# Optimization experiments

Measured on AMD Instinct MI355X. Metric: run time of the kernel, lower is better.

The kernel has to match this reference:

```python
import jax, jax.numpy as jnp
import numpy as np

NUM_HEADS = 12


def setup_inputs() -> dict:
    key = jax.random.key(0)
    ks = jax.random.split(key, 7)
    B, H, W, C = 1, 64, 64, 768
    hd = C // NUM_HEADS
    return {
        "x": jax.random.normal(ks[0], (B, H, W, C), dtype=jnp.float32),
        "qkv_w": jax.random.normal(ks[1], (C, 3 * C), dtype=jnp.float32) * 0.02,
        "qkv_b": jax.random.normal(ks[2], (3 * C,), dtype=jnp.float32) * 0.02,
        "proj_w": jax.random.normal(ks[3], (C, C), dtype=jnp.float32) * 0.02,
        "proj_b": jax.random.normal(ks[4], (C,), dtype=jnp.float32) * 0.02,
        "rel_pos_h": jax.random.normal(ks[5], (2 * H - 1, hd), dtype=jnp.float32) * 0.02,
        "rel_pos_w": jax.random.normal(ks[6], (2 * W - 1, hd), dtype=jnp.float32) * 0.02,
    }


def _rel_table(size, rel_pos):
    # q_size == k_size so relative_coords = i - j + (size - 1)
    coords = jnp.arange(size)[:, None] - jnp.arange(size)[None, :] + (size - 1)
    return rel_pos[coords]  # [size, size, head_dim]


def reference(x, qkv_w, qkv_b, proj_w, proj_b, rel_pos_h, rel_pos_w):
    B, H, W, C = x.shape
    nh = NUM_HEADS
    hd = C // nh
    scale = hd ** -0.5
    N = H * W

    qkv = x.reshape(B, N, C) @ qkv_w + qkv_b  # [B, N, 3C]
    qkv = qkv.reshape(B, N, 3, nh, hd).transpose(2, 0, 3, 1, 4).reshape(3, B * nh, N, hd)
    q, k, v = qkv[0], qkv[1], qkv[2]

    attn = jnp.einsum("bqd,bkd->bqk", q * scale, k)  # [B*nh, N, N]

    # decomposed relative position bias
    Rh = _rel_table(H, rel_pos_h)  # [H, H, hd]
    Rw = _rel_table(W, rel_pos_w)  # [W, W, hd]
    qr = q.reshape(B * nh, H, W, hd)
    rel_h = jnp.einsum("bhwc,hkc->bhwk", qr, Rh)  # [B*nh, H, W, H]
    rel_w = jnp.einsum("bhwc,wkc->bhwk", qr, Rw)  # [B*nh, H, W, W]
    bias = rel_h[..., :, None] + rel_w[..., None, :]  # [B*nh, H, W, H, W]
    attn = attn + bias.reshape(B * nh, N, N)

    attn = jax.nn.softmax(attn, axis=-1)
    out = jnp.einsum("bqk,bkd->bqd", attn, v)  # [B*nh, N, hd]
    out = out.reshape(B, nh, H, W, hd).transpose(0, 2, 3, 1, 4).reshape(B, H, W, C)
    return out @ proj_w + proj_b
```

## Files before the change

kernel.cpp:

```cpp
#include <hip/hip_runtime.h>
#include <math.h>

#define NHEADS 12
#define NTOK 4096
#define LOG2E 1.44269504f

typedef __attribute__((ext_vector_type(8))) short bf8v;
typedef __attribute__((ext_vector_type(4))) float f4v;
typedef __attribute__((ext_vector_type(16))) float f16v;

__device__ __forceinline__ unsigned short f2bf(float f) {
  unsigned int u = __float_as_uint(f);
  u += 0x7fffu + ((u >> 16) & 1u);
  return (unsigned short)(u >> 16);
}
__device__ __forceinline__ bf8v pack8(float4 a, float4 b) {
  bf8v v;
  v[0] = (short)f2bf(a.x); v[1] = (short)f2bf(a.y);
  v[2] = (short)f2bf(a.z); v[3] = (short)f2bf(a.w);
  v[4] = (short)f2bf(b.x); v[5] = (short)f2bf(b.y);
  v[6] = (short)f2bf(b.z); v[7] = (short)f2bf(b.w);
  return v;
}
__device__ __forceinline__ unsigned cvtpk(float lo, float hi) {
  unsigned r;
  asm("v_cvt_pk_bf16_f32 %0, %1, %2" : "=v"(r) : "v"(lo), "v"(hi));
  return r;
}
__device__ __forceinline__ void gload_lds16(const void* g, void* l) {
  __builtin_amdgcn_global_load_lds(
      (const __attribute__((address_space(1))) void*)g,
      (__attribute__((address_space(3))) void*)l, 16, 0, 0);
}

__device__ __forceinline__ void tcvt_body(
    const float* __restrict__ in, short* __restrict__ out, int R, int C,
    int bx, int by, int t, float (*Ts)[65])
{
    const int bc = bx * 64, br = by * 64;
    {
        const int r = t >> 2, c0 = (t & 3) * 16;
        const float* src = in + (size_t)(br + r) * C + bc + c0;
#pragma unroll
        for (int i = 0; i < 4; ++i) {
            float4 a = *(const float4*)(src + 4 * i);
            Ts[r][c0 + 4 * i + 0] = a.x;
            Ts[r][c0 + 4 * i + 1] = a.y;
            Ts[r][c0 + 4 * i + 2] = a.z;
            Ts[r][c0 + 4 * i + 3] = a.w;
        }
    }
    __syncthreads();
    const int c = t >> 2, r0 = (t & 3) * 16;
    short* dst = out + (size_t)(bc + c) * R + br + r0;
#pragma unroll
    for (int p = 0; p < 2; ++p) {
        bf8v v;
#pragma unroll
        for (int i = 0; i < 8; ++i) v[i] = (short)f2bf(Ts[r0 + p * 8 + i][c]);
        *(bf8v*)(dst + p * 8) = v;
    }
}

__global__ __launch_bounds__(256) void prep_kernel(
    const float* __restrict__ x, const float* __restrict__ qkvw,
    const float* __restrict__ pw, short* __restrict__ xh,
    short* __restrict__ wqkvT, short* __restrict__ pwT)
{
    __shared__ float Ts[64][65];
    const int bid = blockIdx.x, t = threadIdx.x;
    if (bid < 1536) {
        const size_t i = ((size_t)bid * 256 + t) * 8;
        float4 a = *(const float4*)(x + i);
        float4 b = *(const float4*)(x + i + 4);
        *(bf8v*)(xh + i) = pack8(a, b);
    } else if (bid < 1968) {
        const int idx = bid - 1536;
        tcvt_body(qkvw, wqkvT, 768, 2304, idx % 36, idx / 36, t, Ts);
    } else {
        const int idx = bid - 1968;
        tcvt_body(pw, pwT, 768, 768, idx % 12, idx / 12, t, Ts);
    }
}

__global__ __launch_bounds__(256) void qkv_mfma_kernel(
    const short* __restrict__ xh, const short* __restrict__ wT,
    const float* __restrict__ bias, short* __restrict__ qbh,
    short* __restrict__ kblk, short* __restrict__ vblk)
{
    __shared__ __align__(16) short As[128 * 32];
    __shared__ __align__(16) short Bs[96 * 32];
    const int t = threadIdx.x;
    const int w = t >> 6, lane = t & 63;
    const int l15 = lane & 15, l4 = lane >> 4;
    const int wr = w >> 1, wc = w & 1;
    const int row0 = blockIdx.y * 128, col0 = blockIdx.x * 96;
    const int ldr = lane >> 2;
    const int ldk = (lane & 3) * 8;

    f4v acc[4][3] = {};
    const short* aBase = xh + (size_t)(row0 + w * 32 + ldr) * 768 + ldk;
    const short* bBase0 = wT + (size_t)(col0 + w * 16 + ldr) * 768 + ldk;
    const short* bBase1 = wT + (size_t)(col0 + 64 + w * 16 + ldr) * 768 + ldk;

    for (int kk = 0; kk < 768; kk += 32) {
        __syncthreads();
#pragma unroll
        for (int c = 0; c < 2; ++c)
            gload_lds16(aBase + (size_t)c * 16 * 768 + kk,
                        &As[(w * 32 + c * 16) * 32]);
        gload_lds16(bBase0 + kk, &Bs[(w * 16) * 32]);
        if (w < 2)
            gload_lds16(bBase1 + kk, &Bs[(64 + w * 16) * 32]);
        __syncthreads();
        bf8v af[4], bg[3];
#pragma unroll
        for (int i = 0; i < 4; ++i)
            af[i] = *(const bf8v*)&As[(wr * 64 + 16 * i + l15) * 32 + l4 * 8];
#pragma unroll
        for (int j = 0; j < 3; ++j)
            bg[j] = *(const bf8v*)&Bs[(wc * 48 + 16 * j + l15) * 32 + l4 * 8];
#pragma unroll
        for (int i = 0; i < 4; ++i)
#pragma unroll
            for (int j = 0; j < 3; ++j)
                acc[i][j] = __builtin_amdgcn_mfma_f32_16x16x32_bf16(
                    af[i], bg[j], acc[i][j], 0, 0, 0);
    }

#pragma unroll
    for (int j = 0; j < 3; ++j) {
        const int n = col0 + wc * 48 + 16 * j + l15;
        const int s = n / 768;
        const int rm = n - s * 768;
        const int h = rm >> 6, d = rm & 63;
        const float bv = bias[n];
        if (s == 2) {
#pragma unroll
            for (int i = 0; i < 4; ++i) {
                const int m = row0 + wr * 64 + 16 * i + l4 * 4;
                short4 pv;
                pv.x = (short)f2bf(acc[i][j][0] + bv);
                pv.y = (short)f2bf(acc[i][j][1] + bv);
                pv.z = (short)f2bf(acc[i][j][2] + bv);
                pv.w = (short)f2bf(acc[i][j][3] + bv);
                *(short4*)(vblk +
                           ((size_t)(h * 256 + (m >> 4)) * 64 + d) * 16 +
                           (m & 15)) = pv;
            }
        } else if (s == 0) {
#pragma unroll
            for (int i = 0; i < 4; ++i) {
                const int m = row0 + wr * 64 + 16 * i + l4 * 4;
#pragma unroll
                for (int r = 0; r < 4; ++r)
                    qbh[((size_t)h * NTOK + m + r) * 64 + d] =
                        (short)f2bf(acc[i][j][r] + bv);
            }
        } else {
#pragma unroll
            for (int i = 0; i < 4; ++i) {
                const int m = row0 + wr * 64 + 16 * i + l4 * 4;
                short* dst = kblk +
                    ((((size_t)(h * 128 + (m >> 5)) * 8 + (d >> 3)) * 32 +
                      (m & 31)) * 8 + (d & 7));
#pragma unroll
                for (int r = 0; r < 4; ++r)
                    dst[r * 8] = (short)f2bf(acc[i][j][r] + bv);
            }
        }
    }
}

union FlashSMem {
    float relHs[64][65];
    float U[128 * 65];
    struct {
        float OEp[64][64];
        float lEp[64];
    };
};

__global__ __launch_bounds__(256, 3) void flash_mfma_kernel(
    const short* __restrict__ qbh, const short* __restrict__ kblk,
    const short* __restrict__ vblk, const float* __restrict__ rpw,
    const float* __restrict__ rph, short* __restrict__ aob)
{
    __shared__ __align__(16) FlashSMem sm;

    const int t = threadIdx.x;
    const int qt = blockIdx.x, head = blockIdx.y;
    const int row0 = qt * 64;
    const int lane = t & 63, w = t >> 6;
    const int qh2 = w & 1, th = w >> 1;
    const int l31 = lane & 31, hf = lane >> 5;
    const size_t hB = (size_t)head * NTOK * 64;
    const float SC = 0.125f * LOG2E;

    const int q = row0 + qh2 * 32 + l31;
    bf8v bQ[4];
    {
        const short* qsrc = qbh + hB + (size_t)q * 64;
#pragma unroll
        for (int ks = 0; ks < 4; ++ks)
            bQ[ks] = *(const bf8v*)(qsrc + ks * 16 + hf * 8);
    }

    const short* kb = kblk + (size_t)head * 262144 + th * 4096 + hf * 256 +
                      (size_t)l31 * 8;
    bf8v kf[2][4];
#pragma unroll
    for (int t32 = 0; t32 < 2; ++t32)
#pragma unroll
        for (int ks = 0; ks < 4; ++ks)
            kf[t32][ks] = *(const bf8v*)(kb + t32 * 2048 + ks * 512);

    const short* vb2 = vblk + ((size_t)head * 256 * 64 + l31) * 16 + hf * 8;

#pragma unroll
    for (int jt2 = 0; jt2 < 2; ++jt2) {
        const int jt = 2 * th + jt2;
        int j = jt * 32 + l31;
        if (j > 126) j = 0;
        const float* asrc = rpw + (size_t)j * 64;
        f16v c = {};
#pragma unroll
        for (int ks = 0; ks < 4; ++ks) {
            float4 u0 = *(const float4*)(asrc + ks * 16 + hf * 8);
            float4 u1 = *(const float4*)(asrc + ks * 16 + hf * 8 + 4);
            c = __builtin_amdgcn_mfma_f32_32x32x16_bf16(
                pack8(u0, u1), bQ[ks], c, 0, 0, 0);
        }
#pragma unroll
        for (int reg = 0; reg < 16; ++reg)
            sm.U[(jt * 32 + (reg & 3) + 8 * (reg >> 2) + 4 * hf) * 65 +
                 qh2 * 32 + l31] = c[reg];
    }
    __syncthreads();
    const int qw = qh2 * 32 + l31;
    float rwf[2][4][4];
#pragma unroll
    for (int t32 = 0; t32 < 2; ++t32)
#pragma unroll
        for (int g = 0; g < 4; ++g) {
            const int kw = t32 * 32 + 8 * g + 4 * hf;
#pragma unroll
            for (int e = 0; e < 4; ++e)
                rwf[t32][g][e] =
                    sm.U[(qw + 63 - kw - e) * 65 + qw] * LOG2E;
        }
    __syncthreads();

    {
        const int kh = th * 32 + l31;
        const float* asrc = rph + (size_t)(qt + 63 - kh) * 64;
        f16v c = {};
#pragma unroll
        for (int ks = 0; ks < 4; ++ks) {
            float4 u0 = *(const float4*)(asrc + ks * 16 + hf * 8);
            float4 u1 = *(const float4*)(asrc + ks * 16 + hf * 8 + 4);
            u0.x *= LOG2E; u0.y *= LOG2E; u0.z *= LOG2E; u0.w *= LOG2E;
            u1.x *= LOG2E; u1.y *= LOG2E; u1.z *= LOG2E; u1.w *= LOG2E;
            c = __builtin_amdgcn_mfma_f32_32x32x16_bf16(
                pack8(u0, u1), bQ[ks], c, 0, 0, 0);
        }
#pragma unroll
        for (int reg = 0; reg < 16; ++reg)
            sm.relHs[th * 32 + (reg & 3) + 8 * (reg >> 2) + 4 * hf]
                    [qh2 * 32 + l31] = c[reg];
    }
    __syncthreads();

    f16v O[2] = {{}, {}};
    float lsum = 0.f;

    for (int it = 0; it < 32; ++it) {
        f16v acc[2] = {{}, {}};
#pragma unroll
        for (int ks = 0; ks < 4; ++ks)
#pragma unroll
            for (int t32 = 0; t32 < 2; ++t32)
                acc[t32] = __builtin_amdgcn_mfma_f32_32x32x16_bf16(
                    kf[t32][ks], bQ[ks], acc[t32], 0, 0, 0);

        {
            const int itn = (it < 31) ? it + 1 : 31;
            const short* kp = kb + (size_t)itn * 8192;
#pragma unroll
            for (int t32 = 0; t32 < 2; ++t32)
#pragma unroll
                for (int ks = 0; ks < 4; ++ks)
                    kf[t32][ks] =
                        *(const bf8v*)(kp + t32 * 2048 + ks * 512);
        }

        bf8v vB[2][2][2];
        {
            const short* vit = vb2 + (size_t)(it * 8 + th * 4) * 64 * 16;
#pragma unroll
            for (int t32 = 0; t32 < 2; ++t32)
#pragma unroll
                for (int ks2 = 0; ks2 < 2; ++ks2)
#pragma unroll
                    for (int nt = 0; nt < 2; ++nt)
                        vB[t32][ks2][nt] = *(const bf8v*)(
                            vit + ((size_t)(t32 * 2 + ks2) * 64 + nt * 32) *
                                      16);
        }

        const float rh = sm.relHs[2 * it + th][qw];

        unsigned xg[2][4], yg[2][4];
#pragma unroll
        for (int t32 = 0; t32 < 2; ++t32) {
            float sub = 0.f;
#pragma unroll
            for (int g = 0; g < 4; ++g) {
                const float e0 = __builtin_amdgcn_exp2f(
                    fmaf(acc[t32][4 * g + 0], SC, rwf[t32][g][0] + rh));
                const float e1 = __builtin_amdgcn_exp2f(
                    fmaf(acc[t32][4 * g + 1], SC, rwf[t32][g][1] + rh));
                const float e2 = __builtin_amdgcn_exp2f(
                    fmaf(acc[t32][4 * g + 2], SC, rwf[t32][g][2] + rh));
                const float e3 = __builtin_amdgcn_exp2f(
                    fmaf(acc[t32][4 * g + 3], SC, rwf[t32][g][3] + rh));
                sub += (e0 + e1) + (e2 + e3);
                xg[t32][g] = cvtpk(e0, e1);
                yg[t32][g] = cvtpk(e2, e3);
            }
            lsum += sub;
        }

#pragma unroll
        for (int t32 = 0; t32 < 2; ++t32)
#pragma unroll
            for (int ks2 = 0; ks2 < 2; ++ks2) {
                auto px = __builtin_amdgcn_permlane32_swap(
                    xg[t32][2 * ks2], xg[t32][2 * ks2 + 1], false, false);
                auto py = __builtin_amdgcn_permlane32_swap(
                    yg[t32][2 * ks2], yg[t32][2 * ks2 + 1], false, false);
                int4 av;
                av.x = (int)px[0];
                av.y = (int)py[0];
                av.z = (int)px[1];
                av.w = (int)py[1];
                union { int4 i; bf8v v; } u; u.i = av;
#pragma unroll
                for (int nt = 0; nt < 2; ++nt)
                    O[nt] = __builtin_amdgcn_mfma_f32_32x32x16_bf16(
                        u.v, vB[t32][ks2][nt], O[nt], 0, 0, 0);
            }
    }

    lsum += __shfl_xor(lsum, 32);
    __syncthreads();
    if (th == 1) {
#pragma unroll
        for (int nt = 0; nt < 2; ++nt)
#pragma unroll
            for (int reg = 0; reg < 16; ++reg) {
                const int qr = (reg & 3) + 8 * (reg >> 2) + 4 * hf;
                sm.OEp[qh2 * 32 + qr][nt * 32 + l31] = O[nt][reg];
            }
        if (lane < 32) sm.lEp[qh2 * 32 + l31] = lsum;
    }
    __syncthreads();
    if (th == 0) {
        lsum += sm.lEp[qh2 * 32 + l31];
        const float linv = 1.0f / lsum;
#pragma unroll
        for (int nt = 0; nt < 2; ++nt)
#pragma unroll
            for (int reg = 0; reg < 16; ++reg) {
                const int qr = (reg & 3) + 8 * (reg >> 2) + 4 * hf;
                const float li = __shfl(linv, qr);
                const float o =
                    O[nt][reg] + sm.OEp[qh2 * 32 + qr][nt * 32 + l31];
                aob[(size_t)(row0 + qh2 * 32 + qr) * 768 + head * 64 +
                    nt * 32 + l31] = (short)f2bf(o * li);
            }
    }
}

__global__ __launch_bounds__(256) void proj_mfma_kernel(
    const short* __restrict__ aoh, const short* __restrict__ pwT,
    const float* __restrict__ bias, float* __restrict__ out)
{
    __shared__ __align__(16) short As[64 * 32];
    __shared__ __align__(16) short Bs[128 * 32];
    const int t = threadIdx.x;
    const int w = t >> 6, lane = t & 63;
    const int l15 = lane & 15, l4 = lane >> 4;
    const int wr = w >> 1, wc = w & 1;
    const int row0 = blockIdx.y * 64, col0 = blockIdx.x * 128;
    const int ldr = lane >> 2;
    const int ldk = (lane & 3) * 8;

    f4v acc[2][4] = {};
    const short* aBase = aoh + (size_t)(row0 + w * 16 + ldr) * 768 + ldk;
    const short* bBase = pwT + (size_t)(col0 + w * 32 + ldr) * 768 + ldk;

    for (int kk = 0; kk < 768; kk += 32) {
        __syncthreads();
        gload_lds16(aBase + kk, &As[(w * 16) * 32]);
#pragma unroll
        for (int c = 0; c < 2; ++c)
            gload_lds16(bBase + (size_t)c * 16 * 768 + kk,
                        &Bs[(w * 32 + c * 16) * 32]);
        __syncthreads();
        bf8v af[2], bg[4];
#pragma unroll
        for (int i = 0; i < 2; ++i)
            af[i] = *(const bf8v*)&As[(wr * 32 + 16 * i + l15) * 32 + l4 * 8];
#pragma unroll
        for (int j = 0; j < 4; ++j)
            bg[j] = *(const bf8v*)&Bs[(wc * 64 + 16 * j + l15) * 32 + l4 * 8];
#pragma unroll
        for (int i = 0; i < 2; ++i)
#pragma unroll
            for (int j = 0; j < 4; ++j)
                acc[i][j] = __builtin_amdgcn_mfma_f32_16x16x32_bf16(
                    af[i], bg[j], acc[i][j], 0, 0, 0);
    }

#pragma unroll
    for (int j = 0; j < 4; ++j) {
        const int n = col0 + wc * 64 + 16 * j + l15;
        const float bv = bias[n];
#pragma unroll
        for (int i = 0; i < 2; ++i) {
            const int m = row0 + wr * 32 + 16 * i + l4 * 4;
#pragma unroll
            for (int r = 0; r < 4; ++r)
                out[(size_t)(m + r) * 768 + n] = acc[i][j][r] + bv;
        }
    }
}

extern "C" void kernel_launch(void* const* d_in, const int* in_sizes, int n_in,
                              void* d_out, int out_size, void* d_ws,
                              size_t ws_size, hipStream_t stream)
{
    (void)in_sizes; (void)n_in; (void)out_size; (void)ws_size;
    const float* x    = (const float*)d_in[0];
    const float* qkvw = (const float*)d_in[1];
    const float* qkvb = (const float*)d_in[2];
    const float* pw   = (const float*)d_in[3];
    const float* pb   = (const float*)d_in[4];
    const float* rph  = (const float*)d_in[5];
    const float* rpw  = (const float*)d_in[6];
    float* out = (float*)d_out;

    const size_t S = (size_t)NHEADS * NTOK * 64;
    short* qbh  = (short*)d_ws;
    short* kblk = qbh + S;
    short* vblk = kblk + S;
    short* xh   = vblk + S;
    short* aob  = xh;
    short* wqkvT = xh + S;
    short* pwT  = wqkvT + (size_t)2304 * 768;

    prep_kernel<<<dim3(2112), 256, 0, stream>>>(x, qkvw, pw, xh, wqkvT, pwT);
    qkv_mfma_kernel<<<dim3(24, 32), 256, 0, stream>>>(xh, wqkvT, qkvb,
                                                      qbh, kblk, vblk);
    flash_mfma_kernel<<<dim3(64, NHEADS), 256, 0, stream>>>(qbh, kblk, vblk,
                                                            rpw, rph, aob);
    proj_mfma_kernel<<<dim3(6, 64), 256, 0, stream>>>(aob, pwT, pb, out);
}
```

Measured before the change: 217.9 us.

## Pack rel-pos-w bias to bf16 pairs, reorder K prefetch, halve proj tile width

The per-lane relative-position-W bias registers in the flash kernel are now stored as packed bf16 pairs, which halves their register footprint, and are unpacked with shifts and masks in the inner loop. The next-iteration K fragment prefetch moves after the V loads. The projection GEMM tile shrinks from 64x128 to 64x64, doubling the grid to fill more CUs. The bias packing lowers the precision of the rel-w bias and adds ALU work per score.

After: 212.1 us. 1.03x faster.

```diff
diff --git a/kernel.cpp b/kernel.cpp
--- a/kernel.cpp
+++ b/kernel.cpp
@@ -21,6 +21,10 @@
   v[4] = (short)f2bf(b.x); v[5] = (short)f2bf(b.y);
   v[6] = (short)f2bf(b.z); v[7] = (short)f2bf(b.w);
   return v;
+}
+__device__ __forceinline__ unsigned pkbf(float hi, float lo) {
+  return __builtin_amdgcn_perm(__float_as_uint(hi) + 0x8000u,
+                               __float_as_uint(lo) + 0x8000u, 0x07060302u);
 }
 __device__ __forceinline__ unsigned cvtpk(float lo, float hi) {
   unsigned r;
@@ -238,16 +242,18 @@
     }
     __syncthreads();
     const int qw = qh2 * 32 + l31;
-    float rwf[2][4][4];
+    uint2 rwp[2][4];
 #pragma unroll
     for (int t32 = 0; t32 < 2; ++t32)
 #pragma unroll
         for (int g = 0; g < 4; ++g) {
             const int kw = t32 * 32 + 8 * g + 4 * hf;
-#pragma unroll
-            for (int e = 0; e < 4; ++e)
-                rwf[t32][g][e] =
-                    sm.U[(qw + 63 - kw - e) * 65 + qw] * LOG2E;
+            const float v0 = sm.U[(qw + 63 - kw) * 65 + qw] * LOG2E;
+            const float v1 = sm.U[(qw + 62 - kw) * 65 + qw] * LOG2E;
+            const float v2 = sm.U[(qw + 61 - kw) * 65 + qw] * LOG2E;
+            const float v3 = sm.U[(qw + 60 - kw) * 65 + qw] * LOG2E;
+            rwp[t32][g].x = pkbf(v1, v0);
+            rwp[t32][g].y = pkbf(v3, v2);
         }
     __syncthreads();
 
@@ -283,17 +289,6 @@
                 acc[t32] = __builtin_amdgcn_mfma_f32_32x32x16_bf16(
                     kf[t32][ks], bQ[ks], acc[t32], 0, 0, 0);
 
-        {
-            const int itn = (it < 31) ? it + 1 : 31;
-            const short* kp = kb + (size_t)itn * 8192;
-#pragma unroll
-            for (int t32 = 0; t32 < 2; ++t32)
-#pragma unroll
-                for (int ks = 0; ks < 4; ++ks)
-                    kf[t32][ks] =
-                        *(const bf8v*)(kp + t32 * 2048 + ks * 512);
-        }
-
         bf8v vB[2][2][2];
         {
             const short* vit = vb2 + (size_t)(it * 8 + th * 4) * 64 * 16;
@@ -308,6 +303,17 @@
                                       16);
         }
 
+        {
+            const int itn = (it < 31) ? it + 1 : 31;
+            const short* kp = kb + (size_t)itn * 8192;
+#pragma unroll
+            for (int t32 = 0; t32 < 2; ++t32)
+#pragma unroll
+                for (int ks = 0; ks < 4; ++ks)
+                    kf[t32][ks] =
+                        *(const bf8v*)(kp + t32 * 2048 + ks * 512);
+        }
+
         const float rh = sm.relHs[2 * it + th][qw];
 
         unsigned xg[2][4], yg[2][4];
@@ -316,14 +322,20 @@
             float sub = 0.f;
 #pragma unroll
             for (int g = 0; g < 4; ++g) {
+                const unsigned u0 = rwp[t32][g].x;
+                const unsigned u1 = rwp[t32][g].y;
+                const float b0 = __uint_as_float(u0 << 16) + rh;
+                const float b1 = __uint_as_float(u0 & 0xffff0000u) + rh;
+                const float b2 = __uint_as_float(u1 << 16) + rh;
+                const float b3 = __uint_as_float(u1 & 0xffff0000u) + rh;
                 const float e0 = __builtin_amdgcn_exp2f(
-                    fmaf(acc[t32][4 * g + 0], SC, rwf[t32][g][0] + rh));
+                    fmaf(acc[t32][4 * g + 0], SC, b0));
                 const float e1 = __builtin_amdgcn_exp2f(
-                    fmaf(acc[t32][4 * g + 1], SC, rwf[t32][g][1] + rh));
+                    fmaf(acc[t32][4 * g + 1], SC, b1));
                 const float e2 = __builtin_amdgcn_exp2f(
-                    fmaf(acc[t32][4 * g + 2], SC, rwf[t32][g][2] + rh));
+                    fmaf(acc[t32][4 * g + 2], SC, b2));
                 const float e3 = __builtin_amdgcn_exp2f(
-                    fmaf(acc[t32][4 * g + 3], SC, rwf[t32][g][3] + rh));
+                    fmaf(acc[t32][4 * g + 3], SC, b3));
                 sub += (e0 + e1) + (e2 + e3);
                 xg[t32][g] = cvtpk(e0, e1);
                 yg[t32][g] = cvtpk(e2, e3);
@@ -387,45 +399,42 @@
     const float* __restrict__ bias, float* __restrict__ out)
 {
     __shared__ __align__(16) short As[64 * 32];
-    __shared__ __align__(16) short Bs[128 * 32];
+    __shared__ __align__(16) short Bs[64 * 32];
     const int t = threadIdx.x;
     const int w = t >> 6, lane = t & 63;
     const int l15 = lane & 15, l4 = lane >> 4;
     const int wr = w >> 1, wc = w & 1;
-    const int row0 = blockIdx.y * 64, col0 = blockIdx.x * 128;
+    const int row0 = blockIdx.y * 64, col0 = blockIdx.x * 64;
     const int ldr = lane >> 2;
     const int ldk = (lane & 3) * 8;
 
-    f4v acc[2][4] = {};
+    f4v acc[2][2] = {};
     const short* aBase = aoh + (size_t)(row0 + w * 16 + ldr) * 768 + ldk;
-    const short* bBase = pwT + (size_t)(col0 + w * 32 + ldr) * 768 + ldk;
+    const short* bBase = pwT + (size_t)(col0 + w * 16 + ldr) * 768 + ldk;
 
     for (int kk = 0; kk < 768; kk += 32) {
         __syncthreads();
         gload_lds16(aBase + kk, &As[(w * 16) * 32]);
-#pragma unroll
-        for (int c = 0; c < 2; ++c)
-            gload_lds16(bBase + (size_t)c * 16 * 768 + kk,
-                        &Bs[(w * 32 + c * 16) * 32]);
+        gload_lds16(bBase + kk, &Bs[(w * 16) * 32]);
         __syncthreads();
-        bf8v af[2], bg[4];
+        bf8v af[2], bg[2];
 #pragma unroll
         for (int i = 0; i < 2; ++i)
             af[i] = *(const bf8v*)&As[(wr * 32 + 16 * i + l15) * 32 + l4 * 8];
 #pragma unroll
-        for (int j = 0; j < 4; ++j)
-            bg[j] = *(const bf8v*)&Bs[(wc * 64 + 16 * j + l15) * 32 + l4 * 8];
+        for (int j = 0; j < 2; ++j)
+            bg[j] = *(const bf8v*)&Bs[(wc * 32 + 16 * j + l15) * 32 + l4 * 8];
 #pragma unroll
         for (int i = 0; i < 2; ++i)
 #pragma unroll
-            for (int j = 0; j < 4; ++j)
+            for (int j = 0; j < 2; ++j)
                 acc[i][j] = __builtin_amdgcn_mfma_f32_16x16x32_bf16(
                     af[i], bg[j], acc[i][j], 0, 0, 0);
     }
 
 #pragma unroll
-    for (int j = 0; j < 4; ++j) {
-        const int n = col0 + wc * 64 + 16 * j + l15;
+    for (int j = 0; j < 2; ++j) {
+        const int n = col0 + wc * 32 + 16 * j + l15;
         const float bv = bias[n];
 #pragma unroll
         for (int i = 0; i < 2; ++i) {
@@ -465,5 +474,5 @@
                                                       qbh, kblk, vblk);
     flash_mfma_kernel<<<dim3(64, NHEADS), 256, 0, stream>>>(qbh, kblk, vblk,
                                                             rpw, rph, aob);
-    proj_mfma_kernel<<<dim3(6, 64), 256, 0, stream>>>(aob, pwT, pb, out);
-}
+    proj_mfma_kernel<<<dim3(12, 64), 256, 0, stream>>>(aob, pwT, pb, out);
+}
```
